# Kernel optimization log

Hardware: AMD Instinct MI355X
Metric: run time of the kernel (lower is better)

The kernel has to match this reference:

```python
import jax, jax.numpy as jnp
import numpy as np

B, T_CACHE, N_STATE, N_HEAD = 128, 448, 1280, 20
HEAD_DIM = N_STATE // N_HEAD


def setup_inputs() -> dict:
    key = jax.random.key(0)
    ks = jax.random.split(key, 10)
    s = 1.0 / np.sqrt(N_STATE)
    return {
        "x": jax.random.normal(ks[0], (B, 1, N_STATE), jnp.float32),
        "k_cache": jax.random.normal(ks[1], (B, T_CACHE, N_STATE), jnp.float32),
        "v_cache": jax.random.normal(ks[2], (B, T_CACHE, N_STATE), jnp.float32),
        "mask": jnp.zeros((1, T_CACHE), jnp.float32),
        "Wq": jax.random.normal(ks[3], (N_STATE, N_STATE), jnp.float32) * s,
        "bq": jax.random.normal(ks[4], (N_STATE,), jnp.float32) * s,
        "Wk": jax.random.normal(ks[5], (N_STATE, N_STATE), jnp.float32) * s,
        "Wv": jax.random.normal(ks[6], (N_STATE, N_STATE), jnp.float32) * s,
        "bv": jax.random.normal(ks[7], (N_STATE,), jnp.float32) * s,
        "Wo": jax.random.normal(ks[8], (N_STATE, N_STATE), jnp.float32) * s,
        "bo": jax.random.normal(ks[9], (N_STATE,), jnp.float32) * s,
    }


def reference(x, k_cache, v_cache, mask, Wq, bq, Wk, Wv, bv, Wo, bo):
    b, q_len, n_state = x.shape  # q_len == 1 in loop (streaming) mode
    h, d = N_HEAD, n_state // N_HEAD

    # Q/K/V projections (Whisper: key has no bias)
    q = x @ Wq + bq                         # [B, 1, n_state]
    k = x @ Wk                              # [B, 1, n_state]
    v = x @ Wv + bv                         # [B, 1, n_state]

    # streaming KV-cache shift-and-append
    k_cache = jnp.concatenate([k_cache[:, 1:, :], k], axis=1)  # [B, T, n_state]
    v_cache = jnp.concatenate([v_cache[:, 1:, :], v], axis=1)

    t = k_cache.shape[1]
    scale = d ** (-0.25)
    qh = q.reshape(b, q_len, h, d).transpose(0, 2, 1, 3) * scale   # [B, H, q, d]
    kh = k_cache.reshape(b, t, h, d).transpose(0, 2, 3, 1) * scale  # [B, H, d, T]
    vh = v_cache.reshape(b, t, h, d).transpose(0, 2, 1, 3)          # [B, H, T, d]

    qk = jnp.matmul(qh, kh) + mask          # [B, H, q, T]
    qk = qk.astype(jnp.float32)
    w = jax.nn.softmax(qk, axis=-1).astype(qh.dtype)
    wv = jnp.matmul(w, vh)                  # [B, H, q, d]
    wv = wv.transpose(0, 2, 1, 3).reshape(b, q_len, n_state)

    out = wv @ Wo + bo                      # [B, q, n_state]
    return out, k_cache, v_cache
```

## Files before the change

kernel.cpp:

```cpp
#include <hip/hip_runtime.h>
#include <cstddef>

#define NSTATE 1280
#define TCACHE 448
#define NBATCH 128
#define NHEAD  20
#define HDIM   64
#define NT     8
#define RPC    (TCACHE / NT)
#define KSPLIT 4
#define KRANGE (NSTATE / KSPLIT)

typedef float f4 __attribute__((ext_vector_type(4)));
typedef float f32x4 __attribute__((ext_vector_type(4)));
typedef short bf16x8 __attribute__((ext_vector_type(8)));
typedef unsigned short u16;
typedef unsigned short u16x8 __attribute__((ext_vector_type(8)));

__device__ __forceinline__ u16 f2bf(float f) {
    unsigned u = __builtin_bit_cast(unsigned, f);
    u += 0x7fff + ((u >> 16) & 1);
    return (u16)(u >> 16);
}

__device__ __forceinline__ void mfma_partial_body(
    const float* __restrict__ A, const float* __restrict__ W,
    float* __restrict__ P)
{
    __shared__ u16 As[128][40];
    __shared__ u16 Bs[64][40];
    const int tid = threadIdx.x;
    const int n0 = blockIdx.x * 64;
    const int kb = blockIdx.y * KRANGE;
    const int w = tid >> 6, l = tid & 63;
    const int la = l & 15, kg = l >> 4;
    const int arow = tid >> 1, akh = (tid & 1) << 4;
    const int bkr = tid >> 3, bnc = (tid & 7) << 3;
    f32x4 acc[8] = {};

    for (int ks = 0; ks < KRANGE; ks += 32) {
        {
            const float* src = A + (size_t)arow * NSTATE + kb + ks + akh;
            float4 v0 = *(const float4*)(src);
            float4 v1 = *(const float4*)(src + 4);
            float4 v2 = *(const float4*)(src + 8);
            float4 v3 = *(const float4*)(src + 12);
            u16x8 w0, w1;
            w0[0]=f2bf(v0.x); w0[1]=f2bf(v0.y); w0[2]=f2bf(v0.z); w0[3]=f2bf(v0.w);
            w0[4]=f2bf(v1.x); w0[5]=f2bf(v1.y); w0[6]=f2bf(v1.z); w0[7]=f2bf(v1.w);
            w1[0]=f2bf(v2.x); w1[1]=f2bf(v2.y); w1[2]=f2bf(v2.z); w1[3]=f2bf(v2.w);
            w1[4]=f2bf(v3.x); w1[5]=f2bf(v3.y); w1[6]=f2bf(v3.z); w1[7]=f2bf(v3.w);
            *(u16x8*)&As[arow][akh]     = w0;
            *(u16x8*)&As[arow][akh + 8] = w1;
        }
        {
            const float* src = W + (size_t)(kb + ks + bkr) * NSTATE + n0 + bnc;
            float4 b0 = *(const float4*)(src);
            float4 b1 = *(const float4*)(src + 4);
            Bs[bnc + 0][bkr] = f2bf(b0.x); Bs[bnc + 1][bkr] = f2bf(b0.y);
            Bs[bnc + 2][bkr] = f2bf(b0.z); Bs[bnc + 3][bkr] = f2bf(b0.w);
            Bs[bnc + 4][bkr] = f2bf(b1.x); Bs[bnc + 5][bkr] = f2bf(b1.y);
            Bs[bnc + 6][bkr] = f2bf(b1.z); Bs[bnc + 7][bkr] = f2bf(b1.w);
        }
        __syncthreads();
        const bf16x8 bf = *(const bf16x8*)&Bs[w * 16 + la][kg * 8];
        #pragma unroll
        for (int mf = 0; mf < 8; ++mf) {
            bf16x8 af = *(const bf16x8*)&As[mf * 16 + la][kg * 8];
            acc[mf] = __builtin_amdgcn_mfma_f32_16x16x32_bf16(af, bf, acc[mf], 0, 0, 0);
        }
        __syncthreads();
    }
    const int col = n0 + w * 16 + la;
    #pragma unroll
    for (int mf = 0; mf < 8; ++mf)
        #pragma unroll
        for (int j = 0; j < 4; ++j)
            P[(size_t)(mf * 16 + kg * 4 + j) * NSTATE + col] = acc[mf][j];
}

__global__ void __launch_bounds__(256) proj_mfma_kernel(
    const float* __restrict__ x,
    const float* __restrict__ Wq, const float* __restrict__ Wk,
    const float* __restrict__ Wv, float* __restrict__ pp)
{
    const int z = blockIdx.z;
    const float* W = (z == 0) ? Wq : (z == 1) ? Wk : Wv;
    mfma_partial_body(x, W,
        pp + (size_t)(z * KSPLIT + blockIdx.y) * NBATCH * NSTATE);
}

__global__ void __launch_bounds__(256) proj_reduce_kernel(
    const float* __restrict__ pp, const float* __restrict__ bq,
    const float* __restrict__ bv, float* __restrict__ q_ws,
    float* __restrict__ kout, float* __restrict__ vout)
{
    const int mat = blockIdx.y;
    const size_t idx = ((size_t)blockIdx.x * 256 + threadIdx.x) * 4;
    const int b = (int)(idx / NSTATE), col = (int)(idx % NSTATE);
    float4 v = make_float4(0.f, 0.f, 0.f, 0.f);
    #pragma unroll
    for (int c = 0; c < KSPLIT; ++c) {
        float4 a = *(const float4*)(pp + (size_t)(mat * KSPLIT + c) * NBATCH * NSTATE + idx);
        v.x += a.x; v.y += a.y; v.z += a.z; v.w += a.w;
    }
    if (mat == 0) {
        float4 bb = *(const float4*)(bq + col);
        v.x = (v.x + bb.x) * 0.125f; v.y = (v.y + bb.y) * 0.125f;
        v.z = (v.z + bb.z) * 0.125f; v.w = (v.w + bb.w) * 0.125f;
        *(float4*)(q_ws + idx) = v;
    } else if (mat == 1) {
        *(float4*)(kout + ((size_t)b * TCACHE + TCACHE - 1) * NSTATE + col) = v;
    } else {
        float4 bb = *(const float4*)(bv + col);
        v.x += bb.x; v.y += bb.y; v.z += bb.z; v.w += bb.w;
        *(float4*)(vout + ((size_t)b * TCACHE + TCACHE - 1) * NSTATE + col) = v;
    }
}

__global__ void __launch_bounds__(320) fused_stream_kernel(
    const float* __restrict__ kin, const float* __restrict__ vin,
    const float* __restrict__ q_ws, const float* __restrict__ mask,
    float* __restrict__ kout, float* __restrict__ vout,
    float* __restrict__ pvp, float* __restrict__ m_ws, float* __restrict__ s_ws)
{
    const int tc = blockIdx.x, b = blockIdx.y;
    const int tid = threadIdx.x;
    const int h = tid >> 4, l = tid & 15;
    const int col = tid << 2;
    const size_t base = (size_t)b * TCACHE * NSTATE;
    const int t0 = tc * RPC;
    const int nrows = (tc == NT - 1) ? RPC - 1 : RPC;

    __shared__ float sc[NHEAD][RPC];

    const float4 q4 = *(const float4*)(q_ws + (size_t)b * NSTATE + col);
    const float* ksrc = kin + base + (size_t)(t0 + 1) * NSTATE + col;
    const float* vsrc = vin + base + (size_t)(t0 + 1) * NSTATE + col;
    float* kdst = kout + base + (size_t)t0 * NSTATE + col;
    float* vdst = vout + base + (size_t)t0 * NSTATE + col;

    {
        int r = 0;
        for (; r + 8 <= nrows; r += 8) {
            f4 kb[8];
            #pragma unroll
            for (int j = 0; j < 8; ++j)
                kb[j] = __builtin_nontemporal_load((const f4*)(ksrc + (size_t)(r + j) * NSTATE));
            #pragma unroll
            for (int j = 0; j < 8; ++j)
                __builtin_nontemporal_store(kb[j], (f4*)(kdst + (size_t)(r + j) * NSTATE));
            #pragma unroll
            for (int j = 0; j < 8; ++j) {
                float p = kb[j][0]*q4.x + kb[j][1]*q4.y + kb[j][2]*q4.z + kb[j][3]*q4.w;
                p += __shfl_xor(p, 1); p += __shfl_xor(p, 2);
                p += __shfl_xor(p, 4); p += __shfl_xor(p, 8);
                if (l == 0) sc[h][r + j] = p + mask[t0 + r + j];
            }
        }
        for (; r < nrows; ++r) {
            f4 kv = __builtin_nontemporal_load((const f4*)(ksrc + (size_t)r * NSTATE));
            __builtin_nontemporal_store(kv, (f4*)(kdst + (size_t)r * NSTATE));
            float p = kv[0]*q4.x + kv[1]*q4.y + kv[2]*q4.z + kv[3]*q4.w;
            p += __shfl_xor(p, 1); p += __shfl_xor(p, 2);
            p += __shfl_xor(p, 4); p += __shfl_xor(p, 8);
            if (l == 0) sc[h][r] = p + mask[t0 + r];
        }
        if (tc == NT - 1) {
            const f4 kv = *(const f4*)(kout + base + (size_t)(TCACHE-1) * NSTATE + col);
            float p = kv[0]*q4.x + kv[1]*q4.y + kv[2]*q4.z + kv[3]*q4.w;
            p += __shfl_xor(p, 1); p += __shfl_xor(p, 2);
            p += __shfl_xor(p, 4); p += __shfl_xor(p, 8);
            if (l == 0) sc[h][RPC - 1] = p + mask[TCACHE - 1];
        }
    }
    __syncthreads();

    {
        float v[4];
        float m = -1e30f;
        #pragma unroll
        for (int j = 0; j < 4; ++j) {
            int r = l + 16 * j;
            v[j] = (r < RPC) ? sc[h][r] : -1e30f;
            m = fmaxf(m, v[j]);
        }
        #pragma unroll
        for (int d = 1; d <= 8; d <<= 1) m = fmaxf(m, __shfl_xor(m, d));
        float s = 0.f;
        #pragma unroll
        for (int j = 0; j < 4; ++j) {
            v[j] = __expf(v[j] - m);
            s += v[j];
        }
        #pragma unroll
        for (int d = 1; d <= 8; d <<= 1) s += __shfl_xor(s, d);
        __syncthreads();
        #pragma unroll
        for (int j = 0; j < 4; ++j) {
            int r = l + 16 * j;
            if (r < RPC) sc[h][r] = v[j];
        }
        if (l == 0) {
            m_ws[((size_t)b * NT + tc) * NHEAD + h] = m;
            s_ws[((size_t)b * NT + tc) * NHEAD + h] = s;
        }
    }
    __syncthreads();

    float ax = 0.f, ay = 0.f, az = 0.f, aw = 0.f;
    {
        int r = 0;
        for (; r + 8 <= nrows; r += 8) {
            f4 vb[8];
            #pragma unroll
            for (int j = 0; j < 8; ++j)
                vb[j] = __builtin_nontemporal_load((const f4*)(vsrc + (size_t)(r + j) * NSTATE));
            #pragma unroll
            for (int j = 0; j < 8; ++j)
                __builtin_nontemporal_store(vb[j], (f4*)(vdst + (size_t)(r + j) * NSTATE));
            #pragma unroll
            for (int j = 0; j < 8; ++j) {
                const float w = sc[h][r + j];
                ax = fmaf(w, vb[j][0], ax); ay = fmaf(w, vb[j][1], ay);
                az = fmaf(w, vb[j][2], az); aw = fmaf(w, vb[j][3], aw);
            }
        }
        for (; r < nrows; ++r) {
            f4 vv = __builtin_nontemporal_load((const f4*)(vsrc + (size_t)r * NSTATE));
            __builtin_nontemporal_store(vv, (f4*)(vdst + (size_t)r * NSTATE));
            const float w = sc[h][r];
            ax = fmaf(w, vv[0], ax); ay = fmaf(w, vv[1], ay);
            az = fmaf(w, vv[2], az); aw = fmaf(w, vv[3], aw);
        }
        if (tc == NT - 1) {
            const f4 vv = *(const f4*)(vout + base + (size_t)(TCACHE-1) * NSTATE + col);
            const float w = sc[h][RPC - 1];
            ax = fmaf(w, vv[0], ax); ay = fmaf(w, vv[1], ay);
            az = fmaf(w, vv[2], az); aw = fmaf(w, vv[3], aw);
        }
    }
    *(float4*)(pvp + ((size_t)b * NT + tc) * NSTATE + col) =
        make_float4(ax, ay, az, aw);
}

__global__ void __launch_bounds__(256) combine_kernel(
    const float* __restrict__ pvp, const float* __restrict__ m_ws,
    const float* __restrict__ s_ws, float* __restrict__ wv_ws)
{
    const size_t idx = ((size_t)blockIdx.x * 256 + threadIdx.x) * 4;
    const int b = (int)(idx / NSTATE), col = (int)(idx % NSTATE);
    const int h = col >> 6;

    float m[NT], s[NT];
    float M = -1e30f;
    #pragma unroll
    for (int c = 0; c < NT; ++c) {
        m[c] = m_ws[((size_t)b * NT + c) * NHEAD + h];
        s[c] = s_ws[((size_t)b * NT + c) * NHEAD + h];
        M = fmaxf(M, m[c]);
    }
    float S = 0.f;
    float f[NT];
    #pragma unroll
    for (int c = 0; c < NT; ++c) { f[c] = __expf(m[c] - M); S += s[c] * f[c]; }
    const float inv = 1.0f / S;

    float4 acc = make_float4(0.f, 0.f, 0.f, 0.f);
    #pragma unroll
    for (int c = 0; c < NT; ++c) {
        const float w = f[c] * inv;
        float4 a = *(const float4*)(pvp + ((size_t)b * NT + c) * NSTATE + col);
        acc.x = fmaf(w, a.x, acc.x); acc.y = fmaf(w, a.y, acc.y);
        acc.z = fmaf(w, a.z, acc.z); acc.w = fmaf(w, a.w, acc.w);
    }
    *(float4*)(wv_ws + idx) = acc;
}

__global__ void __launch_bounds__(256) outproj_mfma_kernel(
    const float* __restrict__ wv, const float* __restrict__ Wo,
    float* __restrict__ po)
{
    mfma_partial_body(wv, Wo, po + (size_t)blockIdx.y * NBATCH * NSTATE);
}

__global__ void __launch_bounds__(256) out_reduce_kernel(
    const float* __restrict__ po, const float* __restrict__ bo,
    float* __restrict__ out)
{
    const size_t idx = ((size_t)blockIdx.x * 256 + threadIdx.x) * 4;
    const int col = (int)(idx % NSTATE);
    float4 s = *(const float4*)(bo + col);
    #pragma unroll
    for (int c = 0; c < KSPLIT; ++c) {
        float4 a = *(const float4*)(po + (size_t)c * NBATCH * NSTATE + idx);
        s.x += a.x; s.y += a.y; s.z += a.z; s.w += a.w;
    }
    *(float4*)(out + idx) = s;
}

extern "C" void kernel_launch(void* const* d_in, const int* in_sizes, int n_in,
                              void* d_out, int out_size, void* d_ws, size_t ws_size,
                              hipStream_t stream)
{
    const float* x       = (const float*)d_in[0];
    const float* k_cache = (const float*)d_in[1];
    const float* v_cache = (const float*)d_in[2];
    const float* mask    = (const float*)d_in[3];
    const float* Wq      = (const float*)d_in[4];
    const float* bq      = (const float*)d_in[5];
    const float* Wk      = (const float*)d_in[6];
    const float* Wv      = (const float*)d_in[7];
    const float* bv      = (const float*)d_in[8];
    const float* Wo      = (const float*)d_in[9];
    const float* bo      = (const float*)d_in[10];

    float* out  = (float*)d_out;
    float* kout = out + (size_t)NBATCH * NSTATE;
    float* vout = kout + (size_t)NBATCH * TCACHE * NSTATE;

    float* ws     = (float*)d_ws;
    float* q_ws   = ws;
    float* pvp_ws = q_ws  + (size_t)NBATCH * NSTATE;
    float* m_ws   = pvp_ws + (size_t)NBATCH * NT * NSTATE;
    float* s_ws   = m_ws  + (size_t)NBATCH * NT * NHEAD;
    float* wv_ws  = s_ws  + (size_t)NBATCH * NT * NHEAD;
    float* pp_ws  = wv_ws + (size_t)NBATCH * NSTATE;
    float* po_ws  = pp_ws + (size_t)3 * KSPLIT * NBATCH * NSTATE;

    proj_mfma_kernel<<<dim3(20, KSPLIT, 3), 256, 0, stream>>>(x, Wq, Wk, Wv, pp_ws);
    proj_reduce_kernel<<<dim3(160, 3), 256, 0, stream>>>(pp_ws, bq, bv,
                                                         q_ws, kout, vout);
    fused_stream_kernel<<<dim3(NT, NBATCH), 320, 0, stream>>>(
        k_cache, v_cache, q_ws, mask, kout, vout, pvp_ws, m_ws, s_ws);
    combine_kernel<<<dim3(160), 256, 0, stream>>>(pvp_ws, m_ws, s_ws, wv_ws);
    outproj_mfma_kernel<<<dim3(20, KSPLIT), 256, 0, stream>>>(wv_ws, Wo, po_ws);
    out_reduce_kernel<<<dim3(160), 256, 0, stream>>>(po_ws, bo, out);
}
```

Baseline: 266.4 us.

## Fuse projection reduce into stream kernel and use two 640-thread chunks per batch

Removes the separate proj_reduce kernel: each stream block now sums the split-K partials for q (and, in one chunk, for the new k/v row) itself, keeping them in shared memory. The time axis is split into 2 chunks of 224 rows instead of 8 chunks of 56. Each block has 640 threads, with two halves handling interleaved rows and adding their partial PV sums through shared memory. The aim is to save a launch plus a global round trip for q and to shrink the combine work. The cost is only 256 blocks in the grid, which may give less memory-level parallelism for a bandwidth-bound copy kernel.

```diff
diff --git a/kernel.cpp b/kernel.cpp
--- a/kernel.cpp
+++ b/kernel.cpp
@@ -6,8 +6,8 @@
 #define NBATCH 128
 #define NHEAD  20
 #define HDIM   64
-#define NT     8
-#define RPC    (TCACHE / NT)
+#define NCH    2
+#define CROWS  (TCACHE / NCH)
 #define KSPLIT 4
 #define KRANGE (NSTATE / KSPLIT)
 
@@ -90,158 +90,163 @@
         pp + (size_t)(z * KSPLIT + blockIdx.y) * NBATCH * NSTATE);
 }
 
-__global__ void __launch_bounds__(256) proj_reduce_kernel(
+__global__ void __launch_bounds__(640) fused_stream_kernel(
+    const float* __restrict__ kin, const float* __restrict__ vin,
     const float* __restrict__ pp, const float* __restrict__ bq,
-    const float* __restrict__ bv, float* __restrict__ q_ws,
-    float* __restrict__ kout, float* __restrict__ vout)
-{
-    const int mat = blockIdx.y;
-    const size_t idx = ((size_t)blockIdx.x * 256 + threadIdx.x) * 4;
-    const int b = (int)(idx / NSTATE), col = (int)(idx % NSTATE);
-    float4 v = make_float4(0.f, 0.f, 0.f, 0.f);
-    #pragma unroll
-    for (int c = 0; c < KSPLIT; ++c) {
-        float4 a = *(const float4*)(pp + (size_t)(mat * KSPLIT + c) * NBATCH * NSTATE + idx);
-        v.x += a.x; v.y += a.y; v.z += a.z; v.w += a.w;
-    }
-    if (mat == 0) {
-        float4 bb = *(const float4*)(bq + col);
-        v.x = (v.x + bb.x) * 0.125f; v.y = (v.y + bb.y) * 0.125f;
-        v.z = (v.z + bb.z) * 0.125f; v.w = (v.w + bb.w) * 0.125f;
-        *(float4*)(q_ws + idx) = v;
-    } else if (mat == 1) {
-        *(float4*)(kout + ((size_t)b * TCACHE + TCACHE - 1) * NSTATE + col) = v;
-    } else {
-        float4 bb = *(const float4*)(bv + col);
-        v.x += bb.x; v.y += bb.y; v.z += bb.z; v.w += bb.w;
-        *(float4*)(vout + ((size_t)b * TCACHE + TCACHE - 1) * NSTATE + col) = v;
-    }
-}
-
-__global__ void __launch_bounds__(320) fused_stream_kernel(
-    const float* __restrict__ kin, const float* __restrict__ vin,
-    const float* __restrict__ q_ws, const float* __restrict__ mask,
+    const float* __restrict__ bv, const float* __restrict__ mask,
     float* __restrict__ kout, float* __restrict__ vout,
     float* __restrict__ pvp, float* __restrict__ m_ws, float* __restrict__ s_ws)
 {
-    const int tc = blockIdx.x, b = blockIdx.y;
+    const int cc = blockIdx.x, b = blockIdx.y;
     const int tid = threadIdx.x;
-    const int h = tid >> 4, l = tid & 15;
-    const int col = tid << 2;
+    const int half = tid >= 320 ? 1 : 0;
+    const int rl = tid - half * 320;
+    const int h = rl >> 4, l = rl & 15;
+    const int col = rl << 2;
     const size_t base = (size_t)b * TCACHE * NSTATE;
-    const int t0 = tc * RPC;
-    const int nrows = (tc == NT - 1) ? RPC - 1 : RPC;
-
-    __shared__ float sc[NHEAD][RPC];
-
-    const float4 q4 = *(const float4*)(q_ws + (size_t)b * NSTATE + col);
-    const float* ksrc = kin + base + (size_t)(t0 + 1) * NSTATE + col;
-    const float* vsrc = vin + base + (size_t)(t0 + 1) * NSTATE + col;
-    float* kdst = kout + base + (size_t)t0 * NSTATE + col;
-    float* vdst = vout + base + (size_t)t0 * NSTATE + col;
+    const int t0 = cc * CROWS;
+
+    __shared__ float qs[NSTATE];
+    __shared__ float sc[NHEAD][CROWS];
+    __shared__ float kv447[2][NSTATE];
+    __shared__ float pvtmp[NSTATE];
+
+    if (tid < 320) {
+        const int c4 = tid << 2;
+        f4 a = {0.f, 0.f, 0.f, 0.f};
+        #pragma unroll
+        for (int c = 0; c < KSPLIT; ++c)
+            a += *(const f4*)(pp + ((size_t)c * NBATCH + b) * NSTATE + c4);
+        a = (a + *(const f4*)(bq + c4)) * 0.125f;
+        *(f4*)&qs[c4] = a;
+    } else if (cc == 1) {
+        const int c4 = (tid - 320) << 2;
+        f4 k = {0.f, 0.f, 0.f, 0.f}, v = {0.f, 0.f, 0.f, 0.f};
+        #pragma unroll
+        for (int c = 0; c < KSPLIT; ++c) {
+            k += *(const f4*)(pp + ((size_t)(KSPLIT + c) * NBATCH + b) * NSTATE + c4);
+            v += *(const f4*)(pp + ((size_t)(2 * KSPLIT + c) * NBATCH + b) * NSTATE + c4);
+        }
+        v += *(const f4*)(bv + c4);
+        *(f4*)&kv447[0][c4] = k;
+        *(f4*)&kv447[1][c4] = v;
+        *(f4*)(kout + base + (size_t)(TCACHE - 1) * NSTATE + c4) = k;
+        *(f4*)(vout + base + (size_t)(TCACHE - 1) * NSTATE + c4) = v;
+    }
+    __syncthreads();
+
+    const f4 q4 = *(const f4*)&qs[col];
+    const int nsteps = (cc == 0) ? CROWS / 2 : (CROWS - 2) / 2;
+    const size_t RS = (size_t)2 * NSTATE;
+    const float* ksrc = kin + base + (size_t)(t0 + 1 + half) * NSTATE + col;
+    const float* vsrc = vin + base + (size_t)(t0 + 1 + half) * NSTATE + col;
+    float* kdst = kout + base + (size_t)(t0 + half) * NSTATE + col;
+    float* vdst = vout + base + (size_t)(t0 + half) * NSTATE + col;
 
     {
-        int r = 0;
-        for (; r + 8 <= nrows; r += 8) {
+        int s = 0;
+        for (; s + 8 <= nsteps; s += 8) {
             f4 kb[8];
             #pragma unroll
             for (int j = 0; j < 8; ++j)
-                kb[j] = __builtin_nontemporal_load((const f4*)(ksrc + (size_t)(r + j) * NSTATE));
-            #pragma unroll
-            for (int j = 0; j < 8; ++j)
-                __builtin_nontemporal_store(kb[j], (f4*)(kdst + (size_t)(r + j) * NSTATE));
+                kb[j] = __builtin_nontemporal_load((const f4*)(ksrc + (size_t)(s + j) * RS));
+            #pragma unroll
+            for (int j = 0; j < 8; ++j)
+                __builtin_nontemporal_store(kb[j], (f4*)(kdst + (size_t)(s + j) * RS));
             #pragma unroll
             for (int j = 0; j < 8; ++j) {
-                float p = kb[j][0]*q4.x + kb[j][1]*q4.y + kb[j][2]*q4.z + kb[j][3]*q4.w;
+                const int r = 2 * (s + j) + half;
+                float p = kb[j][0]*q4[0] + kb[j][1]*q4[1] + kb[j][2]*q4[2] + kb[j][3]*q4[3];
                 p += __shfl_xor(p, 1); p += __shfl_xor(p, 2);
                 p += __shfl_xor(p, 4); p += __shfl_xor(p, 8);
-                if (l == 0) sc[h][r + j] = p + mask[t0 + r + j];
+                if (l == 0) sc[h][r] = p + mask[t0 + r];
             }
         }
-        for (; r < nrows; ++r) {
-            f4 kv = __builtin_nontemporal_load((const f4*)(ksrc + (size_t)r * NSTATE));
-            __builtin_nontemporal_store(kv, (f4*)(kdst + (size_t)r * NSTATE));
-            float p = kv[0]*q4.x + kv[1]*q4.y + kv[2]*q4.z + kv[3]*q4.w;
+        for (; s < nsteps; ++s) {
+            const int r = 2 * s + half;
+            f4 kv = __builtin_nontemporal_load((const f4*)(ksrc + (size_t)s * RS));
+            __builtin_nontemporal_store(kv, (f4*)(kdst + (size_t)s * RS));
+            float p = kv[0]*q4[0] + kv[1]*q4[1] + kv[2]*q4[2] + kv[3]*q4[3];
             p += __shfl_xor(p, 1); p += __shfl_xor(p, 2);
             p += __shfl_xor(p, 4); p += __shfl_xor(p, 8);
             if (l == 0) sc[h][r] = p + mask[t0 + r];
         }
-        if (tc == NT - 1) {
-            const f4 kv = *(const f4*)(kout + base + (size_t)(TCACHE-1) * NSTATE + col);
-            float p = kv[0]*q4.x + kv[1]*q4.y + kv[2]*q4.z + kv[3]*q4.w;
+        if (cc == 1 && !half) {
+            f4 kv = __builtin_nontemporal_load(
+                (const f4*)(kin + base + (size_t)447 * NSTATE + col));
+            __builtin_nontemporal_store(kv,
+                (f4*)(kout + base + (size_t)446 * NSTATE + col));
+            float p = kv[0]*q4[0] + kv[1]*q4[1] + kv[2]*q4[2] + kv[3]*q4[3];
             p += __shfl_xor(p, 1); p += __shfl_xor(p, 2);
             p += __shfl_xor(p, 4); p += __shfl_xor(p, 8);
-            if (l == 0) sc[h][RPC - 1] = p + mask[TCACHE - 1];
+            if (l == 0) sc[h][222] = p + mask[446];
+            const f4 k7 = *(const f4*)&kv447[0][col];
+            float p7 = k7[0]*q4[0] + k7[1]*q4[1] + k7[2]*q4[2] + k7[3]*q4[3];
+            p7 += __shfl_xor(p7, 1); p7 += __shfl_xor(p7, 2);
+            p7 += __shfl_xor(p7, 4); p7 += __shfl_xor(p7, 8);
+            if (l == 0) sc[h][223] = p7 + mask[447];
         }
     }
     __syncthreads();
 
     {
-        float v[4];
+        const int hh = tid >> 5;
+        const int slot = tid & 31;
+        float v[7];
         float m = -1e30f;
         #pragma unroll
-        for (int j = 0; j < 4; ++j) {
-            int r = l + 16 * j;
-            v[j] = (r < RPC) ? sc[h][r] : -1e30f;
-            m = fmaxf(m, v[j]);
-        }
-        #pragma unroll
-        for (int d = 1; d <= 8; d <<= 1) m = fmaxf(m, __shfl_xor(m, d));
+        for (int j = 0; j < 7; ++j) { v[j] = sc[hh][slot + 32 * j]; m = fmaxf(m, v[j]); }
+        #pragma unroll
+        for (int d = 1; d <= 16; d <<= 1) m = fmaxf(m, __shfl_xor(m, d));
         float s = 0.f;
         #pragma unroll
-        for (int j = 0; j < 4; ++j) {
-            v[j] = __expf(v[j] - m);
-            s += v[j];
-        }
-        #pragma unroll
-        for (int d = 1; d <= 8; d <<= 1) s += __shfl_xor(s, d);
-        __syncthreads();
-        #pragma unroll
-        for (int j = 0; j < 4; ++j) {
-            int r = l + 16 * j;
-            if (r < RPC) sc[h][r] = v[j];
-        }
-        if (l == 0) {
-            m_ws[((size_t)b * NT + tc) * NHEAD + h] = m;
-            s_ws[((size_t)b * NT + tc) * NHEAD + h] = s;
+        for (int j = 0; j < 7; ++j) { v[j] = __expf(v[j] - m); s += v[j]; }
+        #pragma unroll
+        for (int d = 1; d <= 16; d <<= 1) s += __shfl_xor(s, d);
+        #pragma unroll
+        for (int j = 0; j < 7; ++j) sc[hh][slot + 32 * j] = v[j];
+        if (slot == 0) {
+            m_ws[((size_t)b * NCH + cc) * NHEAD + hh] = m;
+            s_ws[((size_t)b * NCH + cc) * NHEAD + hh] = s;
         }
     }
     __syncthreads();
 
-    float ax = 0.f, ay = 0.f, az = 0.f, aw = 0.f;
+    f4 acc = {0.f, 0.f, 0.f, 0.f};
     {
-        int r = 0;
-        for (; r + 8 <= nrows; r += 8) {
+        int s = 0;
+        for (; s + 8 <= nsteps; s += 8) {
             f4 vb[8];
             #pragma unroll
             for (int j = 0; j < 8; ++j)
-                vb[j] = __builtin_nontemporal_load((const f4*)(vsrc + (size_t)(r + j) * NSTATE));
-            #pragma unroll
-            for (int j = 0; j < 8; ++j)
-                __builtin_nontemporal_store(vb[j], (f4*)(vdst + (size_t)(r + j) * NSTATE));
-            #pragma unroll
-            for (int j = 0; j < 8; ++j) {
-                const float w = sc[h][r + j];
-                ax = fmaf(w, vb[j][0], ax); ay = fmaf(w, vb[j][1], ay);
-                az = fmaf(w, vb[j][2], az); aw = fmaf(w, vb[j][3], aw);
-            }
-        }
-        for (; r < nrows; ++r) {
-            f4 vv = __builtin_nontemporal_load((const f4*)(vsrc + (size_t)r * NSTATE));
-            __builtin_nontemporal_store(vv, (f4*)(vdst + (size_t)r * NSTATE));
-            const float w = sc[h][r];
-            ax = fmaf(w, vv[0], ax); ay = fmaf(w, vv[1], ay);
-            az = fmaf(w, vv[2], az); aw = fmaf(w, vv[3], aw);
-        }
-        if (tc == NT - 1) {
-            const f4 vv = *(const f4*)(vout + base + (size_t)(TCACHE-1) * NSTATE + col);
-            const float w = sc[h][RPC - 1];
-            ax = fmaf(w, vv[0], ax); ay = fmaf(w, vv[1], ay);
-            az = fmaf(w, vv[2], az); aw = fmaf(w, vv[3], aw);
-        }
-    }
-    *(float4*)(pvp + ((size_t)b * NT + tc) * NSTATE + col) =
-        make_float4(ax, ay, az, aw);
+                vb[j] = __builtin_nontemporal_load((const f4*)(vsrc + (size_t)(s + j) * RS));
+            #pragma unroll
+            for (int j = 0; j < 8; ++j)
+                __builtin_nontemporal_store(vb[j], (f4*)(vdst + (size_t)(s + j) * RS));
+            #pragma unroll
+            for (int j = 0; j < 8; ++j)
+                acc += vb[j] * sc[h][2 * (s + j) + half];
+        }
+        for (; s < nsteps; ++s) {
+            f4 vv = __builtin_nontemporal_load((const f4*)(vsrc + (size_t)s * RS));
+            __builtin_nontemporal_store(vv, (f4*)(vdst + (size_t)s * RS));
+            acc += vv * sc[h][2 * s + half];
+        }
+        if (cc == 1 && !half) {
+            f4 vv = __builtin_nontemporal_load(
+                (const f4*)(vin + base + (size_t)447 * NSTATE + col));
+            __builtin_nontemporal_store(vv,
+                (f4*)(vout + base + (size_t)446 * NSTATE + col));
+            acc += vv * sc[h][222];
+            acc += (*(const f4*)&kv447[1][col]) * sc[h][223];
+        }
+    }
+    if (half) *(f4*)&pvtmp[col] = acc;
+    __syncthreads();
+    if (!half) {
+        f4 o = *(const f4*)&pvtmp[col] + acc;
+        *(f4*)(pvp + ((size_t)b * NCH + cc) * NSTATE + col) = o;
+    }
 }
 
 __global__ void __launch_bounds__(256) combine_kernel(
@@ -252,25 +257,25 @@
     const int b = (int)(idx / NSTATE), col = (int)(idx % NSTATE);
     const int h = col >> 6;
 
-    float m[NT], s[NT];
+    float m[NCH], s[NCH];
     float M = -1e30f;
     #pragma unroll
-    for (int c = 0; c < NT; ++c) {
-        m[c] = m_ws[((size_t)b * NT + c) * NHEAD + h];
-        s[c] = s_ws[((size_t)b * NT + c) * NHEAD + h];
+    for (int c = 0; c < NCH; ++c) {
+        m[c] = m_ws[((size_t)b * NCH + c) * NHEAD + h];
+        s[c] = s_ws[((size_t)b * NCH + c) * NHEAD + h];
         M = fmaxf(M, m[c]);
     }
     float S = 0.f;
-    float f[NT];
-    #pragma unroll
-    for (int c = 0; c < NT; ++c) { f[c] = __expf(m[c] - M); S += s[c] * f[c]; }
+    float f[NCH];
+    #pragma unroll
+    for (int c = 0; c < NCH; ++c) { f[c] = __expf(m[c] - M); S += s[c] * f[c]; }
     const float inv = 1.0f / S;
 
     float4 acc = make_float4(0.f, 0.f, 0.f, 0.f);
     #pragma unroll
-    for (int c = 0; c < NT; ++c) {
+    for (int c = 0; c < NCH; ++c) {
         const float w = f[c] * inv;
-        float4 a = *(const float4*)(pvp + ((size_t)b * NT + c) * NSTATE + col);
+        float4 a = *(const float4*)(pvp + ((size_t)b * NCH + c) * NSTATE + col);
         acc.x = fmaf(w, a.x, acc.x); acc.y = fmaf(w, a.y, acc.y);
         acc.z = fmaf(w, a.z, acc.z); acc.w = fmaf(w, a.w, acc.w);
     }
@@ -320,19 +325,16 @@
     float* vout = kout + (size_t)NBATCH * TCACHE * NSTATE;
 
     float* ws     = (float*)d_ws;
-    float* q_ws   = ws;
-    float* pvp_ws = q_ws  + (size_t)NBATCH * NSTATE;
-    float* m_ws   = pvp_ws + (size_t)NBATCH * NT * NSTATE;
-    float* s_ws   = m_ws  + (size_t)NBATCH * NT * NHEAD;
-    float* wv_ws  = s_ws  + (size_t)NBATCH * NT * NHEAD;
+    float* pvp_ws = ws;
+    float* m_ws   = pvp_ws + (size_t)NBATCH * NCH * NSTATE;
+    float* s_ws   = m_ws  + (size_t)NBATCH * NCH * NHEAD;
+    float* wv_ws  = s_ws  + (size_t)NBATCH * NCH * NHEAD;
     float* pp_ws  = wv_ws + (size_t)NBATCH * NSTATE;
     float* po_ws  = pp_ws + (size_t)3 * KSPLIT * NBATCH * NSTATE;
 
     proj_mfma_kernel<<<dim3(20, KSPLIT, 3), 256, 0, stream>>>(x, Wq, Wk, Wv, pp_ws);
-    proj_reduce_kernel<<<dim3(160, 3), 256, 0, stream>>>(pp_ws, bq, bv,
-                                                         q_ws, kout, vout);
-    fused_stream_kernel<<<dim3(NT, NBATCH), 320, 0, stream>>>(
-        k_cache, v_cache, q_ws, mask, kout, vout, pvp_ws, m_ws, s_ws);
+    fused_stream_kernel<<<dim3(NCH, NBATCH), 640, 0, stream>>>(
+        k_cache, v_cache, pp_ws, bq, bv, mask, kout, vout, pvp_ws, m_ws, s_ws);
     combine_kernel<<<dim3(160), 256, 0, stream>>>(pvp_ws, m_ws, s_ws, wv_ws);
     outproj_mfma_kernel<<<dim3(20, KSPLIT), 256, 0, stream>>>(wv_ws, Wo, po_ws);
     out_reduce_kernel<<<dim3(160), 256, 0, stream>>>(po_ws, bo, out);
```

Result: slower. 280.3 us (+5.2%).
